# Kernel optimization log

Hardware: AMD Instinct MI355X
Metric: run time of the kernel (lower is better)

## Reference

```python
import jax, jax.numpy as jnp
import numpy as np

TAU = 0.8
V_TH = 0.5
W_D1_GPI = -0.8
W_D2_STN = 0.5
W_STN_GPI = 0.6
GPI_TONIC = 0.4
NOISE = 0.1
T, B = 512, 256
N_D1, N_D2, N_GPI, N_STN = 128, 128, 64, 64


def setup_inputs() -> dict:
    key = jax.random.key(0)
    ks = jax.random.split(key, 7)
    return {
        "x": jax.random.normal(ks[0], (T, B, 2), dtype=jnp.float32),
        "dopa": jax.random.uniform(ks[1], (T, B), dtype=jnp.float32),
        "rpe": jax.random.normal(ks[2], (T, B), dtype=jnp.float32),
        "W_d1": jax.random.normal(ks[3], (N_D1, 2), dtype=jnp.float32) * 0.5,
        "W_d2": jax.random.normal(ks[4], (N_D2, 2), dtype=jnp.float32) * 0.5,
        "noise_d1": jax.random.normal(ks[5], (T, B, N_D1), dtype=jnp.float32),
        "noise_d2": jax.random.normal(ks[6], (T, B, N_D2), dtype=jnp.float32),
    }


def reference(x, dopa, rpe, W_d1, W_d2, noise_d1, noise_d2):
    """Runs T LIF steps of the spiking basal-ganglia circuit for B circuits.

    Returns gates [T, B] = d1_rate - gpi_rate per step. rpe is unused (as in source).
    """
    dt = x.dtype
    v0 = (
        jnp.zeros((B, N_D1), dt),
        jnp.zeros((B, N_D2), dt),
        jnp.zeros((B, N_GPI), dt),
        jnp.zeros((B, N_STN), dt),
    )

    def lif(v, I):
        v = TAU * v + (1.0 - TAU) * I
        s = (v >= V_TH).astype(dt)
        return v * (1.0 - s), s

    def step(carry, inp):
        v_d1, v_d2, v_gpi, v_stn = carry
        xt, dop, nd1, nd2 = inp  # [B,2], [B], [B,N], [B,N]
        d1_mod = (1.0 + dop * 0.5)[:, None]
        d2_mod = (1.0 - dop * 0.3)[:, None]
        I_d1 = jnp.einsum("bi,ni->bn", xt, W_d1) * d1_mod
        v_d1, s_d1 = lif(v_d1, I_d1 + nd1 * NOISE)
        I_d2 = jnp.einsum("bi,ni->bn", xt, W_d2) * d2_mod
        v_d2, s_d2 = lif(v_d2, I_d2 + nd2 * NOISE)
        I_stn = (s_d2.mean(axis=1) * W_D2_STN)[:, None]  # [B,1] broadcast to [B,N_STN]
        v_stn, s_stn = lif(v_stn, I_stn)
        I_gpi = (GPI_TONIC + s_d1.mean(axis=1) * W_D1_GPI + s_stn.mean(axis=1) * W_STN_GPI)[:, None]
        v_gpi, s_gpi = lif(v_gpi, I_gpi)
        gate = s_d1.mean(axis=1) - s_gpi.mean(axis=1)  # [B]
        return (v_d1, v_d2, v_gpi, v_stn), gate

    _, gates = jax.lax.scan(step, v0, (x, dopa, noise_d1, noise_d2))
    return gates  # [T, B]
```

## Files before the change

### kernel.cpp

```cpp
#include <hip/hip_runtime.h>


__global__ __launch_bounds__(576, 1) void bg_kernel(
    const float* __restrict__ x,
    const float* __restrict__ dopa,
    const float* __restrict__ Wd1,
    const float* __restrict__ Wd2,
    const float* __restrict__ nd1,
    const float* __restrict__ nd2,
    float* __restrict__ out)
{
#pragma clang fp contract(off)
    constexpr int T = 512, B = 256;
    constexpr int S = 32;
    constexpr int NCH = T / S;
    constexpr size_t TSTRIDE = (size_t)B * 128;

    __shared__ float lds_I[3][S][64][4];
    __shared__ float lds_x[T][2];
    __shared__ float lds_d[T];

    const int b    = blockIdx.x;
    const int tid  = threadIdx.x;
    const int wv   = tid >> 6;
    const int lane = tid & 63;

    for (int t = tid; t < T; t += 576) {
        const float2 xv = *(const float2*)(x + (size_t)t * (B * 2) + b * 2);
        lds_x[t][0] = xv.x;
        lds_x[t][1] = xv.y;
        lds_d[t]    = dopa[(size_t)t * B + b];
    }
    __syncthreads();

    if (wv == 0) {
        __syncthreads();

        float v1a = 0.0f, v1b = 0.0f;
        float v2a = 0.0f, v2b = 0.0f;
        float v_stn = 0.0f, v_gpi = 0.0f;
        float gate_reg = 0.0f;

        for (int i = 0; i < NCH; ++i) {
            const float (*buf)[64][4] = lds_I[i % 3];

#pragma unroll
            for (int s = 0; s < S; ++s) {
                const float4 I = *(const float4*)&buf[s][lane][0];

                v1a = 0.8f * v1a + 0.2f * I.x;
                v1b = 0.8f * v1b + 0.2f * I.y;
                v2a = 0.8f * v2a + 0.2f * I.z;
                v2b = 0.8f * v2b + 0.2f * I.w;

                const bool s1a = v1a >= 0.5f, s1b = v1b >= 0.5f;
                const bool s2a = v2a >= 0.5f, s2b = v2b >= 0.5f;
                v1a = s1a ? 0.0f : v1a;
                v1b = s1b ? 0.0f : v1b;
                v2a = s2a ? 0.0f : v2a;
                v2b = s2b ? 0.0f : v2b;

                const int c1 = __popcll(__ballot(s1a)) + __popcll(__ballot(s1b));
                const int c2 = __popcll(__ballot(s2a)) + __popcll(__ballot(s2b));
                const float mean1 = (float)c1 * 0.0078125f;
                const float mean2 = (float)c2 * 0.0078125f;

                const float I_stn = mean2 * 0.5f;
                v_stn = 0.8f * v_stn + 0.2f * I_stn;
                const float s_stn = (v_stn >= 0.5f) ? 1.0f : 0.0f;
                v_stn = (v_stn >= 0.5f) ? 0.0f : v_stn;

                const float I_gpi = (0.4f + mean1 * -0.8f) + s_stn * 0.6f;
                v_gpi = 0.8f * v_gpi + 0.2f * I_gpi;
                const float s_gpi = (v_gpi >= 0.5f) ? 1.0f : 0.0f;
                v_gpi = (v_gpi >= 0.5f) ? 0.0f : v_gpi;

                const float gate = mean1 - s_gpi;

                const int latch = ((i & 1) << 5) | s;
                gate_reg = (lane == latch) ? gate : gate_reg;
            }

            if (i & 1) {
                const int t0 = (i - 1) * S;
                out[(size_t)(t0 + lane) * B + b] = gate_reg;
            }

            __syncthreads();
        }
    } else {
        const float4 w1 = *(const float4*)(Wd1 + 4 * lane);
        const float4 w2 = *(const float4*)(Wd2 + 4 * lane);
        const float* n1b = nd1 + (size_t)b * 128 + 2 * lane;
        const float* n2b = nd2 + (size_t)b * 128 + 2 * lane;
        const int p0 = (wv - 1) * 4;

        auto stage = [&](int c, int bf) {
            const int tbase = c * S;
            float2 a1[4], a2[4];
#pragma unroll
            for (int j = 0; j < 4; ++j) {
                const int t = tbase + p0 + j;
                a1[j] = *(const float2*)(n1b + (size_t)t * TSTRIDE);
                a2[j] = *(const float2*)(n2b + (size_t)t * TSTRIDE);
            }
#pragma unroll
            for (int j = 0; j < 4; ++j) {
                const int s = p0 + j;
                const int t = tbase + s;
                const float xx = lds_x[t][0], xy = lds_x[t][1];
                const float dop = lds_d[t];

                const float m1 = 1.0f + dop * 0.5f;
                const float m2 = 1.0f - dop * 0.3f;

                const float dot1a = __builtin_fmaf(xy, w1.y, xx * w1.x);
                const float dot1b = __builtin_fmaf(xy, w1.w, xx * w1.z);
                const float dot2a = __builtin_fmaf(xy, w2.y, xx * w2.x);
                const float dot2b = __builtin_fmaf(xy, w2.w, xx * w2.z);

                float4 I;
                I.x = dot1a * m1 + a1[j].x * 0.1f;
                I.y = dot1b * m1 + a1[j].y * 0.1f;
                I.z = dot2a * m2 + a2[j].x * 0.1f;
                I.w = dot2b * m2 + a2[j].y * 0.1f;

                *(float4*)&lds_I[bf][s][lane][0] = I;
            }
        };

        stage(0, 0);
        stage(1, 1);
        __syncthreads();

        for (int i = 0; i < NCH; ++i) {
            if (i + 2 < NCH) stage(i + 2, (i + 2) % 3);
            __syncthreads();
        }
    }
}

extern "C" void kernel_launch(void* const* d_in, const int* in_sizes, int n_in,
                              void* d_out, int out_size, void* d_ws, size_t ws_size,
                              hipStream_t stream) {
    const float* x    = (const float*)d_in[0];
    const float* dopa = (const float*)d_in[1];
    const float* Wd1  = (const float*)d_in[3];
    const float* Wd2  = (const float*)d_in[4];
    const float* nd1  = (const float*)d_in[5];
    const float* nd2  = (const float*)d_in[6];
    float* out = (float*)d_out;

    bg_kernel<<<dim3(256), dim3(576), 0, stream>>>(x, dopa, Wd1, Wd2, nd1, nd2, out);
}
```

Measured before the change: 192.7 us.

## Prefetch noise four chunks ahead in registers and double-buffer LDS

New measurement: 239.0 us. 24.0% more time.

```diff
diff --git a/kernel.cpp b/kernel.cpp
--- a/kernel.cpp
+++ b/kernel.cpp
@@ -16,7 +16,7 @@
     constexpr int NCH = T / S;
     constexpr size_t TSTRIDE = (size_t)B * 128;
 
-    __shared__ float lds_I[3][S][64][4];
+    __shared__ float lds_I[2][S][64][4];
     __shared__ float lds_x[T][2];
     __shared__ float lds_d[T];
 
@@ -42,7 +42,7 @@
         float gate_reg = 0.0f;
 
         for (int i = 0; i < NCH; ++i) {
-            const float (*buf)[64][4] = lds_I[i % 3];
+            const float (*buf)[64][4] = lds_I[i & 1];
 
 #pragma unroll
             for (int s = 0; s < S; ++s) {
@@ -95,48 +95,64 @@
         const float* n2b = nd2 + (size_t)b * 128 + 2 * lane;
         const int p0 = (wv - 1) * 4;
 
-        auto stage = [&](int c, int bf) {
-            const int tbase = c * S;
-            float2 a1[4], a2[4];
+        float2 r1[4][4], r2[4][4];
+
+#define LOADC(c, st)                                                         \
+        if ((c) < NCH) {                                                     \
+            _Pragma("unroll")                                                \
+            for (int j = 0; j < 4; ++j) {                                    \
+                const size_t toff = (size_t)((c) * S + p0 + j) * TSTRIDE;    \
+                r1[st][j] = *(const float2*)(n1b + toff);                    \
+                r2[st][j] = *(const float2*)(n2b + toff);                    \
+            }                                                                \
+        }
+
+#define COMPC(c, st, bf)                                                     \
+        if ((c) < NCH) {                                                     \
+            _Pragma("unroll")                                                \
+            for (int j = 0; j < 4; ++j) {                                    \
+                const int s = p0 + j;                                        \
+                const int t = (c) * S + s;                                   \
+                const float xx = lds_x[t][0], xy = lds_x[t][1];              \
+                const float dop = lds_d[t];                                  \
+                const float m1 = 1.0f + dop * 0.5f;                          \
+                const float m2 = 1.0f - dop * 0.3f;                          \
+                const float dot1a = __builtin_fmaf(xy, w1.y, xx * w1.x);     \
+                const float dot1b = __builtin_fmaf(xy, w1.w, xx * w1.z);     \
+                const float dot2a = __builtin_fmaf(xy, w2.y, xx * w2.x);     \
+                const float dot2b = __builtin_fmaf(xy, w2.w, xx * w2.z);     \
+                float4 I;                                                    \
+                I.x = dot1a * m1 + r1[st][j].x * 0.1f;                       \
+                I.y = dot1b * m1 + r1[st][j].y * 0.1f;                       \
+                I.z = dot2a * m2 + r2[st][j].x * 0.1f;                       \
+                I.w = dot2b * m2 + r2[st][j].y * 0.1f;                       \
+                *(float4*)&lds_I[bf][s][lane][0] = I;                        \
+            }                                                                \
+        }
+
+#define PBAR                                                                 \
+        __builtin_amdgcn_sched_barrier(0);                                   \
+        asm volatile("s_waitcnt lgkmcnt(0)" ::: "memory");                   \
+        __builtin_amdgcn_sched_barrier(0);                                   \
+        __builtin_amdgcn_s_barrier();                                        \
+        __builtin_amdgcn_sched_barrier(0);
+
+        LOADC(0, 0)
+        LOADC(1, 1)
+        LOADC(2, 2)
+        LOADC(3, 3)
+        COMPC(0, 0, 0)
+        PBAR
+
 #pragma unroll
-            for (int j = 0; j < 4; ++j) {
-                const int t = tbase + p0 + j;
-                a1[j] = *(const float2*)(n1b + (size_t)t * TSTRIDE);
-                a2[j] = *(const float2*)(n2b + (size_t)t * TSTRIDE);
-            }
-#pragma unroll
-            for (int j = 0; j < 4; ++j) {
-                const int s = p0 + j;
-                const int t = tbase + s;
-                const float xx = lds_x[t][0], xy = lds_x[t][1];
-                const float dop = lds_d[t];
-
-                const float m1 = 1.0f + dop * 0.5f;
-                const float m2 = 1.0f - dop * 0.3f;
-
-                const float dot1a = __builtin_fmaf(xy, w1.y, xx * w1.x);
-                const float dot1b = __builtin_fmaf(xy, w1.w, xx * w1.z);
-                const float dot2a = __builtin_fmaf(xy, w2.y, xx * w2.x);
-                const float dot2b = __builtin_fmaf(xy, w2.w, xx * w2.z);
-
-                float4 I;
-                I.x = dot1a * m1 + a1[j].x * 0.1f;
-                I.y = dot1b * m1 + a1[j].y * 0.1f;
-                I.z = dot2a * m2 + a2[j].x * 0.1f;
-                I.w = dot2b * m2 + a2[j].y * 0.1f;
-
-                *(float4*)&lds_I[bf][s][lane][0] = I;
-            }
-        };
-
-        stage(0, 0);
-        stage(1, 1);
-        __syncthreads();
-
         for (int i = 0; i < NCH; ++i) {
-            if (i + 2 < NCH) stage(i + 2, (i + 2) % 3);
-            __syncthreads();
+            LOADC(i + 4, (i + 4) & 3)
+            COMPC(i + 1, (i + 1) & 3, (i + 1) & 1)
+            PBAR
         }
+#undef LOADC
+#undef COMPC
+#undef PBAR
     }
 }
 
```

## Offload STN/GPi recurrence to a dedicated wavefront via packed spike counts in LDS

Applied to the files above, without the earlier changes.

Result: no change. 189.0 us (-1.9%).

```diff
diff --git a/kernel.cpp b/kernel.cpp
--- a/kernel.cpp
+++ b/kernel.cpp
@@ -1,7 +1,7 @@
 #include <hip/hip_runtime.h>
 
 
-__global__ __launch_bounds__(576, 1) void bg_kernel(
+__global__ __launch_bounds__(640, 1) void bg_kernel(
     const float* __restrict__ x,
     const float* __restrict__ dopa,
     const float* __restrict__ Wd1,
@@ -19,13 +19,14 @@
     __shared__ float lds_I[3][S][64][4];
     __shared__ float lds_x[T][2];
     __shared__ float lds_d[T];
+    __shared__ unsigned int cnt_lds[2][64];
 
     const int b    = blockIdx.x;
     const int tid  = threadIdx.x;
     const int wv   = tid >> 6;
     const int lane = tid & 63;
 
-    for (int t = tid; t < T; t += 576) {
+    for (int t = tid; t < T; t += 640) {
         const float2 xv = *(const float2*)(x + (size_t)t * (B * 2) + b * 2);
         lds_x[t][0] = xv.x;
         lds_x[t][1] = xv.y;
@@ -38,57 +39,52 @@
 
         float v1a = 0.0f, v1b = 0.0f;
         float v2a = 0.0f, v2b = 0.0f;
-        float v_stn = 0.0f, v_gpi = 0.0f;
-        float gate_reg = 0.0f;
+        unsigned int cnt_reg = 0u;
 
         for (int i = 0; i < NCH; ++i) {
             const float (*buf)[64][4] = lds_I[i % 3];
 
 #pragma unroll
-            for (int s = 0; s < S; ++s) {
-                const float4 I = *(const float4*)&buf[s][lane][0];
+            for (int g = 0; g < 4; ++g) {
+                float4 P[8];
+#pragma unroll
+                for (int k = 0; k < 8; ++k)
+                    P[k] = *(const float4*)&buf[g * 8 + k][lane][0];
 
-                v1a = 0.8f * v1a + 0.2f * I.x;
-                v1b = 0.8f * v1b + 0.2f * I.y;
-                v2a = 0.8f * v2a + 0.2f * I.z;
-                v2b = 0.8f * v2b + 0.2f * I.w;
+#pragma unroll
+                for (int k = 0; k < 8; ++k) {
+                    const int s = g * 8 + k;
+                    const float4 I = P[k];
 
-                const bool s1a = v1a >= 0.5f, s1b = v1b >= 0.5f;
-                const bool s2a = v2a >= 0.5f, s2b = v2b >= 0.5f;
-                v1a = s1a ? 0.0f : v1a;
-                v1b = s1b ? 0.0f : v1b;
-                v2a = s2a ? 0.0f : v2a;
-                v2b = s2b ? 0.0f : v2b;
+                    v1a = 0.8f * v1a + 0.2f * I.x;
+                    v1b = 0.8f * v1b + 0.2f * I.y;
+                    v2a = 0.8f * v2a + 0.2f * I.z;
+                    v2b = 0.8f * v2b + 0.2f * I.w;
 
-                const int c1 = __popcll(__ballot(s1a)) + __popcll(__ballot(s1b));
-                const int c2 = __popcll(__ballot(s2a)) + __popcll(__ballot(s2b));
-                const float mean1 = (float)c1 * 0.0078125f;
-                const float mean2 = (float)c2 * 0.0078125f;
+                    const bool s1a = v1a >= 0.5f, s1b = v1b >= 0.5f;
+                    const bool s2a = v2a >= 0.5f, s2b = v2b >= 0.5f;
+                    v1a = s1a ? 0.0f : v1a;
+                    v1b = s1b ? 0.0f : v1b;
+                    v2a = s2a ? 0.0f : v2a;
+                    v2b = s2b ? 0.0f : v2b;
 
-                const float I_stn = mean2 * 0.5f;
-                v_stn = 0.8f * v_stn + 0.2f * I_stn;
-                const float s_stn = (v_stn >= 0.5f) ? 1.0f : 0.0f;
-                v_stn = (v_stn >= 0.5f) ? 0.0f : v_stn;
+                    const int c1 = __popcll(__ballot(s1a)) + __popcll(__ballot(s1b));
+                    const int c2 = __popcll(__ballot(s2a)) + __popcll(__ballot(s2b));
 
-                const float I_gpi = (0.4f + mean1 * -0.8f) + s_stn * 0.6f;
-                v_gpi = 0.8f * v_gpi + 0.2f * I_gpi;
-                const float s_gpi = (v_gpi >= 0.5f) ? 1.0f : 0.0f;
-                v_gpi = (v_gpi >= 0.5f) ? 0.0f : v_gpi;
-
-                const float gate = mean1 - s_gpi;
-
-                const int latch = ((i & 1) << 5) | s;
-                gate_reg = (lane == latch) ? gate : gate_reg;
+                    const unsigned int packed =
+                        (unsigned int)c1 | ((unsigned int)c2 << 8);
+                    const int latch = ((i & 1) << 5) | s;
+                    cnt_reg = (lane == latch) ? packed : cnt_reg;
+                }
             }
 
             if (i & 1) {
-                const int t0 = (i - 1) * S;
-                out[(size_t)(t0 + lane) * B + b] = gate_reg;
+                cnt_lds[(i >> 1) & 1][lane] = cnt_reg;
             }
 
             __syncthreads();
         }
-    } else {
+    } else if (wv <= 8) {
         const float4 w1 = *(const float4*)(Wd1 + 4 * lane);
         const float4 w2 = *(const float4*)(Wd2 + 4 * lane);
         const float* n1b = nd1 + (size_t)b * 128 + 2 * lane;
@@ -137,6 +133,44 @@
             if (i + 2 < NCH) stage(i + 2, (i + 2) % 3);
             __syncthreads();
         }
+    } else {
+        __syncthreads();
+
+        float v_stn = 0.0f, v_gpi = 0.0f;
+
+        auto process_pair = [&](int p) {
+            const unsigned int cnts = cnt_lds[p & 1][lane];
+            const float mean1v = (float)(int)(cnts & 0xffu) * 0.0078125f;
+            const float mean2v = (float)(int)(cnts >> 8) * 0.0078125f;
+
+            float gate_reg = 0.0f;
+#pragma unroll
+            for (int j = 0; j < 64; ++j) {
+                const float mean1 = __shfl(mean1v, j);
+                const float mean2 = __shfl(mean2v, j);
+
+                const float I_stn = mean2 * 0.5f;
+                v_stn = 0.8f * v_stn + 0.2f * I_stn;
+                const float s_stn = (v_stn >= 0.5f) ? 1.0f : 0.0f;
+                v_stn = (v_stn >= 0.5f) ? 0.0f : v_stn;
+
+                const float I_gpi = (0.4f + mean1 * -0.8f) + s_stn * 0.6f;
+                v_gpi = 0.8f * v_gpi + 0.2f * I_gpi;
+                const float s_gpi = (v_gpi >= 0.5f) ? 1.0f : 0.0f;
+                v_gpi = (v_gpi >= 0.5f) ? 0.0f : v_gpi;
+
+                const float gate = mean1 - s_gpi;
+
+                gate_reg = (lane == j) ? gate : gate_reg;
+            }
+            out[(size_t)(p * 64 + lane) * B + b] = gate_reg;
+        };
+
+        for (int i = 0; i < NCH; ++i) {
+            if (i >= 2 && (i & 1) == 0) process_pair((i >> 1) - 1);
+            __syncthreads();
+        }
+        process_pair(7);
     }
 }
 
@@ -151,5 +185,5 @@
     const float* nd2  = (const float*)d_in[6];
     float* out = (float*)d_out;
 
-    bg_kernel<<<dim3(256), dim3(576), 0, stream>>>(x, dopa, Wd1, Wd2, nd1, nd2, out);
+    bg_kernel<<<dim3(256), dim3(640), 0, stream>>>(x, dopa, Wd1, Wd2, nd1, nd2, out);
 }
```

## Pack four circuits per block with four consumer waves and contiguous noise loads

Applied to the files above, without the earlier changes.

New measurement: 244.6 us. 1.27x slower.

```diff
diff --git a/kernel.cpp b/kernel.cpp
--- a/kernel.cpp
+++ b/kernel.cpp
@@ -1,7 +1,7 @@
 #include <hip/hip_runtime.h>
 
 
-__global__ __launch_bounds__(576, 1) void bg_kernel(
+__global__ __launch_bounds__(768, 1) void bg_kernel(
     const float* __restrict__ x,
     const float* __restrict__ dopa,
     const float* __restrict__ Wd1,
@@ -12,28 +12,30 @@
 {
 #pragma clang fp contract(off)
     constexpr int T = 512, B = 256;
-    constexpr int S = 32;
+    constexpr int S = 16;
     constexpr int NCH = T / S;
-    constexpr size_t TSTRIDE = (size_t)B * 128;
 
-    __shared__ float lds_I[3][S][64][4];
-    __shared__ float lds_x[T][2];
-    __shared__ float lds_d[T];
+    __shared__ float lds_I[2][S][4][64][4];
+    __shared__ float lds_x[T][4][2];
+    __shared__ float lds_d[T][4];
 
-    const int b    = blockIdx.x;
+    const int g    = blockIdx.x;
     const int tid  = threadIdx.x;
     const int wv   = tid >> 6;
     const int lane = tid & 63;
+    const int bc0  = g * 4;
 
-    for (int t = tid; t < T; t += 576) {
-        const float2 xv = *(const float2*)(x + (size_t)t * (B * 2) + b * 2);
-        lds_x[t][0] = xv.x;
-        lds_x[t][1] = xv.y;
-        lds_d[t]    = dopa[(size_t)t * B + b];
+    for (int idx = tid; idx < T * 4; idx += 768) {
+        const int t = idx >> 2, c = idx & 3;
+        const float2 xv = *(const float2*)(x + (size_t)t * (B * 2) + (bc0 + c) * 2);
+        lds_x[t][c][0] = xv.x;
+        lds_x[t][c][1] = xv.y;
+        lds_d[t][c]    = dopa[(size_t)t * B + bc0 + c];
     }
     __syncthreads();
 
-    if (wv == 0) {
+    if (wv < 4) {
+        const int c = wv;
         __syncthreads();
 
         float v1a = 0.0f, v1b = 0.0f;
@@ -42,11 +44,11 @@
         float gate_reg = 0.0f;
 
         for (int i = 0; i < NCH; ++i) {
-            const float (*buf)[64][4] = lds_I[i % 3];
+            const float (*buf)[4][64][4] = lds_I[i & 1];
 
 #pragma unroll
             for (int s = 0; s < S; ++s) {
-                const float4 I = *(const float4*)&buf[s][lane][0];
+                const float4 I = *(const float4*)&buf[s][c][lane][0];
 
                 v1a = 0.8f * v1a + 0.2f * I.x;
                 v1b = 0.8f * v1b + 0.2f * I.y;
@@ -77,64 +79,89 @@
 
                 const float gate = mean1 - s_gpi;
 
-                const int latch = ((i & 1) << 5) | s;
+                const int latch = ((i & 3) << 4) | s;
                 gate_reg = (lane == latch) ? gate : gate_reg;
             }
 
-            if (i & 1) {
-                const int t0 = (i - 1) * S;
-                out[(size_t)(t0 + lane) * B + b] = gate_reg;
+            if ((i & 3) == 3) {
+                const int t0 = (i - 3) * S;
+                out[(size_t)(t0 + lane) * B + bc0 + c] = gate_reg;
             }
 
             __syncthreads();
         }
     } else {
-        const float4 w1 = *(const float4*)(Wd1 + 4 * lane);
-        const float4 w2 = *(const float4*)(Wd2 + 4 * lane);
-        const float* n1b = nd1 + (size_t)b * 128 + 2 * lane;
-        const float* n2b = nd2 + (size_t)b * 128 + 2 * lane;
-        const int p0 = (wv - 1) * 4;
+        const int p  = wv - 4;
+        const int a  = p & 1;
+        const int tg = p >> 1;
+        const float* na = a ? nd2 : nd1;
+        const float* Wa = a ? Wd2 : Wd1;
 
-        auto stage = [&](int c, int bf) {
-            const int tbase = c * S;
-            float2 a1[4], a2[4];
+        const int m  = lane & 15;
+        const int cL = lane >> 4;
+
+        const float4 W0 = *(const float4*)(Wa + 16 * m + 0);
+        const float4 W1 = *(const float4*)(Wa + 16 * m + 4);
+        const float4 W2 = *(const float4*)(Wa + 16 * m + 8);
+        const float4 W3 = *(const float4*)(Wa + 16 * m + 12);
+
+        auto stage = [&](int ch, int bf) {
+            float4 n0[4], n1[4];
 #pragma unroll
             for (int j = 0; j < 4; ++j) {
-                const int t = tbase + p0 + j;
-                a1[j] = *(const float2*)(n1b + (size_t)t * TSTRIDE);
-                a2[j] = *(const float2*)(n2b + (size_t)t * TSTRIDE);
+                const int t = ch * S + tg * 4 + j;
+                const float* src = na + ((size_t)t * B + bc0) * 128 + 8 * lane;
+                n0[j] = *(const float4*)(src);
+                n1[j] = *(const float4*)(src + 4);
             }
 #pragma unroll
             for (int j = 0; j < 4; ++j) {
-                const int s = p0 + j;
-                const int t = tbase + s;
-                const float xx = lds_x[t][0], xy = lds_x[t][1];
-                const float dop = lds_d[t];
+                const int s = tg * 4 + j;
+                const int t = ch * S + s;
+                const float xx  = lds_x[t][cL][0], xy = lds_x[t][cL][1];
+                const float dop = lds_d[t][cL];
+                const float mod = a ? (1.0f - dop * 0.3f) : (1.0f + dop * 0.5f);
 
-                const float m1 = 1.0f + dop * 0.5f;
-                const float m2 = 1.0f - dop * 0.3f;
-
-                const float dot1a = __builtin_fmaf(xy, w1.y, xx * w1.x);
-                const float dot1b = __builtin_fmaf(xy, w1.w, xx * w1.z);
-                const float dot2a = __builtin_fmaf(xy, w2.y, xx * w2.x);
-                const float dot2b = __builtin_fmaf(xy, w2.w, xx * w2.z);
-
-                float4 I;
-                I.x = dot1a * m1 + a1[j].x * 0.1f;
-                I.y = dot1b * m1 + a1[j].y * 0.1f;
-                I.z = dot2a * m2 + a2[j].x * 0.1f;
-                I.w = dot2b * m2 + a2[j].y * 0.1f;
-
-                *(float4*)&lds_I[bf][s][lane][0] = I;
+                {
+                    const float dA = __builtin_fmaf(xy, W0.y, xx * W0.x);
+                    const float dB = __builtin_fmaf(xy, W0.w, xx * W0.z);
+                    float2 o;
+                    o.x = dA * mod + n0[j].x * 0.1f;
+                    o.y = dB * mod + n0[j].y * 0.1f;
+                    *(float2*)&lds_I[bf][s][cL][4 * m + 0][2 * a] = o;
+                }
+                {
+                    const float dA = __builtin_fmaf(xy, W1.y, xx * W1.x);
+                    const float dB = __builtin_fmaf(xy, W1.w, xx * W1.z);
+                    float2 o;
+                    o.x = dA * mod + n0[j].z * 0.1f;
+                    o.y = dB * mod + n0[j].w * 0.1f;
+                    *(float2*)&lds_I[bf][s][cL][4 * m + 1][2 * a] = o;
+                }
+                {
+                    const float dA = __builtin_fmaf(xy, W2.y, xx * W2.x);
+                    const float dB = __builtin_fmaf(xy, W2.w, xx * W2.z);
+                    float2 o;
+                    o.x = dA * mod + n1[j].x * 0.1f;
+                    o.y = dB * mod + n1[j].y * 0.1f;
+                    *(float2*)&lds_I[bf][s][cL][4 * m + 2][2 * a] = o;
+                }
+                {
+                    const float dA = __builtin_fmaf(xy, W3.y, xx * W3.x);
+                    const float dB = __builtin_fmaf(xy, W3.w, xx * W3.z);
+                    float2 o;
+                    o.x = dA * mod + n1[j].z * 0.1f;
+                    o.y = dB * mod + n1[j].w * 0.1f;
+                    *(float2*)&lds_I[bf][s][cL][4 * m + 3][2 * a] = o;
+                }
             }
         };
 
         stage(0, 0);
-        stage(1, 1);
         __syncthreads();
 
         for (int i = 0; i < NCH; ++i) {
-            if (i + 2 < NCH) stage(i + 2, (i + 2) % 3);
+            if (i + 1 < NCH) stage(i + 1, (i + 1) & 1);
             __syncthreads();
         }
     }
@@ -151,5 +178,5 @@
     const float* nd2  = (const float*)d_in[6];
     float* out = (float*)d_out;
 
-    bg_kernel<<<dim3(256), dim3(576), 0, stream>>>(x, dopa, Wd1, Wd2, nd1, nd2, out);
+    bg_kernel<<<dim3(64), dim3(768), 0, stream>>>(x, dopa, Wd1, Wd2, nd1, nd2, out);
 }
```
